# Optimization experiments

Measured on AMD Instinct MI355X. Metric: run time of the kernel, lower is better.

## Reference

```python
import jax, jax.numpy as jnp
import numpy as np

N_NODES = 50000
N_EDGES = 300000
NODE_DIM = 11
EDGE_DIM = 5
HID = 256
L = 4
G = 1024  # num graphs
BN_EPS = 1e-5


def setup_inputs() -> dict:
    key = jax.random.key(0)
    ks = jax.random.split(key, 24)
    s = 0.05
    inp = {
        "x": jax.random.normal(ks[0], (N_NODES, NODE_DIM), jnp.float32),
        "edge_index": jax.random.randint(ks[1], (2, N_EDGES), 0, N_NODES, jnp.int32),
        "edge_attr": jax.random.normal(ks[2], (N_EDGES, EDGE_DIM), jnp.float32),
        "batch": jnp.sort(jax.random.randint(ks[3], (N_NODES,), 0, G, jnp.int32)),
        # node encoder
        "enc_W": jax.random.normal(ks[4], (NODE_DIM, HID), jnp.float32) * s,
        "enc_b": jnp.zeros((HID,), jnp.float32),
        # per-layer GINE params (stacked over layers)
        "edge_W": jax.random.normal(ks[5], (L, EDGE_DIM, HID), jnp.float32) * s,
        "edge_b": jnp.zeros((L, HID), jnp.float32),
        "mlp_W1": jax.random.normal(ks[6], (L, HID, HID), jnp.float32) * s,
        "mlp_b1": jnp.zeros((L, HID), jnp.float32),
        "mlp_W2": jax.random.normal(ks[7], (L, HID, HID), jnp.float32) * s,
        "mlp_b2": jnp.zeros((L, HID), jnp.float32),
        "bn_g": jnp.ones((L, HID), jnp.float32),
        "bn_b": jnp.zeros((L, HID), jnp.float32),
        # head: 3*HID -> HID -> HID//2 -> 1
        "head_W1": jax.random.normal(ks[8], (3 * HID, HID), jnp.float32) * s,
        "head_b1": jnp.zeros((HID,), jnp.float32),
        "head_W2": jax.random.normal(ks[9], (HID, HID // 2), jnp.float32) * s,
        "head_b2": jnp.zeros((HID // 2,), jnp.float32),
        "head_W3": jax.random.normal(ks[10], (HID // 2, 1), jnp.float32) * s,
        "head_b3": jnp.zeros((1,), jnp.float32),
    }
    return inp


def _forward(x, edge_attr, enc_W, enc_b, edge_W, edge_b, mlp_W1, mlp_b1,
             mlp_W2, mlp_b2, bn_g, bn_b, head_W1, head_b1, head_W2, head_b2,
             head_W3, head_b3, edge_index, batch):
    n = x.shape[0]
    src, dst = edge_index[0], edge_index[1]  # messages flow src(j) -> dst(i)
    h = jax.nn.relu(x @ enc_W + enc_b)  # [N, HID]
    for l in range(L):
        e = edge_attr @ edge_W[l] + edge_b[l]                 # [E, HID]
        msg = jax.nn.relu(h[src] + e)                         # [E, HID]
        aggr = jax.ops.segment_sum(msg, dst, num_segments=n)  # [N, HID]
        z = h + aggr                                          # (1+eps)*h + aggr, eps=0
        z = jax.nn.relu(z @ mlp_W1[l] + mlp_b1[l]) @ mlp_W2[l] + mlp_b2[l]
        # BatchNorm over node dim (batch statistics)
        mu = jnp.mean(z, axis=0)
        var = jnp.var(z, axis=0)
        z = (z - mu) * jax.lax.rsqrt(var + BN_EPS) * bn_g[l] + bn_b[l]
        h = jax.nn.relu(z) + h  # residual
    # mean / add / max pooling per graph
    sums = jax.ops.segment_sum(h, batch, num_segments=G)      # [G, HID]
    cnt = jax.ops.segment_sum(jnp.ones((n, 1), h.dtype), batch, num_segments=G)
    mean = sums / jnp.maximum(cnt, 1.0)
    mx = jax.ops.segment_max(h, batch, num_segments=G)
    g = jnp.concatenate([mean, sums, mx], axis=1)             # [G, 3*HID]
    g = jax.nn.relu(g @ head_W1 + head_b1)
    g = jax.nn.relu(g @ head_W2 + head_b2)
    out = g @ head_W3 + head_b3
    return out.reshape(-1)  # [G]


def reference(x, edge_index, edge_attr, batch, enc_W, enc_b, edge_W, edge_b,
              mlp_W1, mlp_b1, mlp_W2, mlp_b2, bn_g, bn_b, head_W1, head_b1,
              head_W2, head_b2, head_W3, head_b3):
    return _forward(x, edge_attr, enc_W, enc_b, edge_W, edge_b, mlp_W1, mlp_b1,
                    mlp_W2, mlp_b2, bn_g, bn_b, head_W1, head_b1, head_W2,
                    head_b2, head_W3, head_b3, edge_index, batch)
```

## Files before the change

### kernel.cpp

```cpp
#include <hip/hip_runtime.h>

#define N_NODES 50000
#define N_EDGES 300000
#define G_GRAPHS 1024
#define HID 256
#define NLAYERS 4

typedef unsigned short ushort_t;
typedef __attribute__((ext_vector_type(8))) short bf16x8;
typedef __attribute__((ext_vector_type(8))) unsigned short u16x8;
typedef __attribute__((ext_vector_type(4))) float f32x4;

__device__ __forceinline__ float bf2f(ushort_t u) {
  unsigned int x = ((unsigned int)u) << 16;
  return __builtin_bit_cast(float, x);
}
__device__ __forceinline__ ushort_t f2bf(float f) {
  unsigned int x = __builtin_bit_cast(unsigned int, f);
  unsigned int lsb = (x >> 16) & 1u;
  x += 0x7fffu + lsb;
  return (ushort_t)(x >> 16);
}

__global__ __launch_bounds__(256) void k_encoder(const float* __restrict__ x,
    const float* __restrict__ W, const float* __restrict__ b,
    ushort_t* __restrict__ h, int n)
{
  int j = threadIdx.x;
  float wcol[11];
#pragma unroll
  for (int k = 0; k < 11; ++k) wcol[k] = W[k * HID + j];
  float bj = b[j];
  __shared__ float xs[8][11];
  int base = blockIdx.x * 8;
  if (j < 88) {
    int r = j / 11, k = j % 11;
    int row = base + r;
    if (row < n) xs[r][k] = x[row * 11 + k];
  }
  __syncthreads();
#pragma unroll
  for (int r = 0; r < 8; ++r) {
    int row = base + r;
    if (row >= n) break;
    float acc = bj;
#pragma unroll
    for (int k = 0; k < 11; ++k) acc += xs[r][k] * wcol[k];
    h[(size_t)row * HID + j] = f2bf(fmaxf(acc, 0.f));
  }
}

__global__ __launch_bounds__(256) void k_hist(const int* __restrict__ dst,
    int* __restrict__ offs, int E)
{
  int e = blockIdx.x * 256 + threadIdx.x;
  if (e < E) atomicAdd(&offs[dst[e]], 1);
}

__global__ __launch_bounds__(1024) void k_scanA(int* __restrict__ offs,
    int* __restrict__ btot, int n)
{
  __shared__ int wsum[16];
  int tid = threadIdx.x, lane = tid & 63, wid = tid >> 6;
  int idx = blockIdx.x * 1024 + tid;
  int v = (idx < n) ? offs[idx] : 0;
  int x = v;
#pragma unroll
  for (int off = 1; off < 64; off <<= 1) {
    int t = __shfl_up(x, off);
    if (lane >= off) x += t;
  }
  if (lane == 63) wsum[wid] = x;
  __syncthreads();
  if (wid == 0 && lane < 16) {
    int w = wsum[lane];
#pragma unroll
    for (int off = 1; off < 16; off <<= 1) {
      int t = __shfl_up(w, off);
      if (lane >= off) w += t;
    }
    wsum[lane] = w;
  }
  __syncthreads();
  int wbase = (wid == 0) ? 0 : wsum[wid - 1];
  if (idx < n) offs[idx] = wbase + x - v;
  if (tid == 0) btot[blockIdx.x] = wsum[15];
}

__global__ __launch_bounds__(64) void k_scanB(int* __restrict__ btot, int nb)
{
  int lane = threadIdx.x;
  int v = (lane < nb) ? btot[lane] : 0;
  int x = v;
#pragma unroll
  for (int off = 1; off < 64; off <<= 1) {
    int t = __shfl_up(x, off);
    if (lane >= off) x += t;
  }
  if (lane < nb) btot[lane] = x - v;
}

__global__ __launch_bounds__(1024) void k_scanC(int* __restrict__ offs,
    const int* __restrict__ btot, int n)
{
  int idx = blockIdx.x * 1024 + threadIdx.x;
  if (idx < n) offs[idx] += btot[blockIdx.x];
}

__global__ __launch_bounds__(256) void k_fill(const int* __restrict__ src,
    const int* __restrict__ dst, int* __restrict__ offs,
    int* __restrict__ esrc, ushort_t* __restrict__ eab,
    const float* __restrict__ ea, int E)
{
  int e = blockIdx.x * 256 + threadIdx.x;
  if (e < E) {
    int d = dst[e];
    int p = atomicAdd(&offs[d], 1);
    esrc[p] = src[e];
    const float* ep = ea + (size_t)e * 5;
    ushort4 lo = make_ushort4(f2bf(ep[0]), f2bf(ep[1]), f2bf(ep[2]), f2bf(ep[3]));
    ushort4 hi = make_ushort4(f2bf(ep[4]), 0, 0, 0);
    *(ushort4*)&eab[(size_t)p * 8] = lo;
    *(ushort4*)&eab[(size_t)p * 8 + 4] = hi;
  }
}

__global__ __launch_bounds__(256) void k_prep(const float* __restrict__ W,
    ushort_t* __restrict__ Wt)
{
  __shared__ float ld[16][257];
  int mat = blockIdx.y;
  int k0 = blockIdx.x * 16;
  const float* Wm = W + (size_t)mat * HID * HID;
  ushort_t* Wtm = Wt + (size_t)mat * HID * HID;
  int tid = threadIdx.x;
#pragma unroll
  for (int i = 0; i < 16; ++i) ld[i][tid] = Wm[(size_t)(k0 + i) * HID + tid];
  __syncthreads();
#pragma unroll
  for (int v = 0; v < 4; ++v) {
    ushort4 u = make_ushort4(f2bf(ld[v*4+0][tid]), f2bf(ld[v*4+1][tid]),
                             f2bf(ld[v*4+2][tid]), f2bf(ld[v*4+3][tid]));
    *(ushort4*)&Wtm[(size_t)tid * HID + k0 + v * 4] = u;
  }
}

__global__ __launch_bounds__(256) void k_prept(const float* __restrict__ W,
    ushort_t* __restrict__ Wt, int K, int N)
{
  int idx = blockIdx.x * 256 + threadIdx.x;
  if (idx >= K * N) return;
  int n = idx / K, k = idx % K;
  Wt[idx] = f2bf(W[(size_t)k * N + n]);
}

struct ev5 { ushort_t s0, s1, s2, s3, s4; };

__device__ __forceinline__ void edge_step(ev5 ev, ushort4 hv,
    const float4& w0, const float4& w1, const float4& w2, const float4& w3,
    const float4& w4, const float4& bi,
    float& ax, float& ay, float& az, float& aw)
{
  float v0 = bf2f(ev.s0), v1 = bf2f(ev.s1), v2 = bf2f(ev.s2),
        v3 = bf2f(ev.s3), v4 = bf2f(ev.s4);
  float m0 = bi.x, m1 = bi.y, m2 = bi.z, m3 = bi.w;
  m0 = fmaf(v0, w0.x, m0); m1 = fmaf(v0, w0.y, m1);
  m2 = fmaf(v0, w0.z, m2); m3 = fmaf(v0, w0.w, m3);
  m0 = fmaf(v1, w1.x, m0); m1 = fmaf(v1, w1.y, m1);
  m2 = fmaf(v1, w1.z, m2); m3 = fmaf(v1, w1.w, m3);
  m0 = fmaf(v2, w2.x, m0); m1 = fmaf(v2, w2.y, m1);
  m2 = fmaf(v2, w2.z, m2); m3 = fmaf(v2, w2.w, m3);
  m0 = fmaf(v3, w3.x, m0); m1 = fmaf(v3, w3.y, m1);
  m2 = fmaf(v3, w3.z, m2); m3 = fmaf(v3, w3.w, m3);
  m0 = fmaf(v4, w4.x, m0); m1 = fmaf(v4, w4.y, m1);
  m2 = fmaf(v4, w4.z, m2); m3 = fmaf(v4, w4.w, m3);
  m0 += bf2f(hv.x); m1 += bf2f(hv.y); m2 += bf2f(hv.z); m3 += bf2f(hv.w);
  ax += fmaxf(m0, 0.f); ay += fmaxf(m1, 0.f);
  az += fmaxf(m2, 0.f); aw += fmaxf(m3, 0.f);
}

__global__ __launch_bounds__(256) void k_gather(const ushort_t* __restrict__ h,
    const int* __restrict__ offs, const int* __restrict__ esrc,
    const ushort_t* __restrict__ eab, const float* __restrict__ eW,
    const float* __restrict__ eb, ushort_t* __restrict__ zin,
    float* __restrict__ stats, int n)
{
  int tid = threadIdx.x;
  if (blockIdx.x == 0) { stats[tid] = 0.f; stats[HID + tid] = 0.f; }
  int wave = tid >> 6, lane = tid & 63;
  int node = blockIdx.x * 4 + wave;
  int c4 = lane * 4;
  float4 w0 = *(const float4*)&eW[0 * HID + c4];
  float4 w1 = *(const float4*)&eW[1 * HID + c4];
  float4 w2 = *(const float4*)&eW[2 * HID + c4];
  float4 w3 = *(const float4*)&eW[3 * HID + c4];
  float4 w4 = *(const float4*)&eW[4 * HID + c4];
  float4 bi = *(const float4*)&eb[c4];
  if (node >= n) return;
  int lo = (node == 0) ? 0 : offs[node - 1];
  int hi = offs[node];
  ushort4 ho = *(const ushort4*)&h[(size_t)node * HID + c4];
  float ax = bf2f(ho.x), ay = bf2f(ho.y), az = bf2f(ho.z), aw = bf2f(ho.w);
  int p = lo;
  for (; p + 3 < hi; p += 4) {
    int s0 = esrc[p], s1 = esrc[p + 1], s2 = esrc[p + 2], s3 = esrc[p + 3];
    ev5 ea0 = *(const ev5*)&eab[(size_t)(p + 0) * 8];
    ev5 ea1 = *(const ev5*)&eab[(size_t)(p + 1) * 8];
    ev5 ea2 = *(const ev5*)&eab[(size_t)(p + 2) * 8];
    ev5 ea3 = *(const ev5*)&eab[(size_t)(p + 3) * 8];
    ushort4 h0 = *(const ushort4*)&h[(size_t)s0 * HID + c4];
    ushort4 h1 = *(const ushort4*)&h[(size_t)s1 * HID + c4];
    ushort4 h2 = *(const ushort4*)&h[(size_t)s2 * HID + c4];
    ushort4 h3 = *(const ushort4*)&h[(size_t)s3 * HID + c4];
    edge_step(ea0, h0, w0, w1, w2, w3, w4, bi, ax, ay, az, aw);
    edge_step(ea1, h1, w0, w1, w2, w3, w4, bi, ax, ay, az, aw);
    edge_step(ea2, h2, w0, w1, w2, w3, w4, bi, ax, ay, az, aw);
    edge_step(ea3, h3, w0, w1, w2, w3, w4, bi, ax, ay, az, aw);
  }
  for (; p < hi; ++p) {
    int s0 = esrc[p];
    ev5 ea0 = *(const ev5*)&eab[(size_t)p * 8];
    ushort4 h0 = *(const ushort4*)&h[(size_t)s0 * HID + c4];
    edge_step(ea0, h0, w0, w1, w2, w3, w4, bi, ax, ay, az, aw);
  }
  *(ushort4*)&zin[(size_t)node * HID + c4] =
      make_ushort4(f2bf(ax), f2bf(ay), f2bf(az), f2bf(aw));
}

__global__ __launch_bounds__(512, 1) void k_mlp(const ushort_t* __restrict__ A,
    const ushort_t* __restrict__ Wt1, const float* __restrict__ b1,
    const ushort_t* __restrict__ Wt2, const float* __restrict__ b2,
    ushort_t* __restrict__ out, float* __restrict__ stats, int M)
{
  __shared__ alignas(16) ushort_t w2L[65536];
  __shared__ alignas(16) ushort_t z1s[2][16 * 264];
  int tid = threadIdx.x;
  int wave = tid >> 6, lane = tid & 63;
  int m = lane & 15, quad = lane >> 4;
  int col0 = wave * 32;
  for (int c = tid; c < 8192; c += 512) {
    int f = c >> 6, l = c & 63;
    int ctg = f >> 3, kt = f & 7;
    int n = ctg * 16 + (l & 15);
    int k = kt * 32 + (l >> 4) * 8;
    *(u16x8*)&w2L[f * 512 + l * 8] = *(const u16x8*)(Wt2 + (size_t)n * HID + k);
  }
  bf16x8 w1f[2][8];
#pragma unroll
  for (int ct = 0; ct < 2; ++ct)
#pragma unroll
    for (int kt = 0; kt < 8; ++kt)
      w1f[ct][kt] = *(const bf16x8*)(
          Wt1 + (size_t)(col0 + ct * 16 + m) * HID + kt * 32 + quad * 8);
  float bv1[2] = {b1[col0 + m], b1[col0 + 16 + m]};
  float bv2[2] = {b2[col0 + m], b2[col0 + 16 + m]};
  float csum[2] = {0.f, 0.f}, csq[2] = {0.f, 0.f};
  int ntiles = M >> 4;
  int parity = 0;
  int ctg0 = wave * 2, ctg1 = wave * 2 + 1;
  __syncthreads();
  int t = blockIdx.x;
  bf16x8 af[8];
  if (t < ntiles) {
    const ushort_t* Ap = A + (size_t)(t * 16 + m) * HID + quad * 8;
#pragma unroll
    for (int kt = 0; kt < 8; ++kt) af[kt] = *(const bf16x8*)(Ap + kt * 32);
  }
  for (; t < ntiles; t += gridDim.x) {
    f32x4 a0 = (f32x4){0.f, 0.f, 0.f, 0.f};
    f32x4 a1 = (f32x4){0.f, 0.f, 0.f, 0.f};
#pragma unroll
    for (int kt = 0; kt < 8; ++kt) {
      a0 = __builtin_amdgcn_mfma_f32_16x16x32_bf16(af[kt], w1f[0][kt], a0, 0, 0, 0);
      a1 = __builtin_amdgcn_mfma_f32_16x16x32_bf16(af[kt], w1f[1][kt], a1, 0, 0, 0);
    }
    ushort_t* buf = z1s[parity];
#pragma unroll
    for (int reg = 0; reg < 4; ++reg) {
      int r = quad * 4 + reg;
      buf[r * 264 + col0 + m]      = f2bf(fmaxf(a0[reg] + bv1[0], 0.f));
      buf[r * 264 + col0 + 16 + m] = f2bf(fmaxf(a1[reg] + bv1[1], 0.f));
    }
    int tn = t + gridDim.x;
    bf16x8 afn[8];
    if (tn < ntiles) {
      const ushort_t* Ap = A + (size_t)(tn * 16 + m) * HID + quad * 8;
#pragma unroll
      for (int kt = 0; kt < 8; ++kt) afn[kt] = *(const bf16x8*)(Ap + kt * 32);
    }
    __syncthreads();
    f32x4 c0 = (f32x4){0.f, 0.f, 0.f, 0.f};
    f32x4 c1 = (f32x4){0.f, 0.f, 0.f, 0.f};
#pragma unroll
    for (int kt = 0; kt < 8; ++kt) {
      bf16x8 zf = *(const bf16x8*)&buf[m * 264 + kt * 32 + quad * 8];
      bf16x8 b0 = *(const bf16x8*)&w2L[(ctg0 * 8 + kt) * 512 + lane * 8];
      bf16x8 b1r = *(const bf16x8*)&w2L[(ctg1 * 8 + kt) * 512 + lane * 8];
      c0 = __builtin_amdgcn_mfma_f32_16x16x32_bf16(zf, b0, c0, 0, 0, 0);
      c1 = __builtin_amdgcn_mfma_f32_16x16x32_bf16(zf, b1r, c1, 0, 0, 0);
    }
    int rb = t * 16 + quad * 4;
#pragma unroll
    for (int reg = 0; reg < 4; ++reg) {
      float o0 = c0[reg] + bv2[0];
      float o1 = c1[reg] + bv2[1];
      out[(size_t)(rb + reg) * HID + col0 + m] = f2bf(o0);
      out[(size_t)(rb + reg) * HID + col0 + 16 + m] = f2bf(o1);
      csum[0] += o0; csq[0] = fmaf(o0, o0, csq[0]);
      csum[1] += o1; csq[1] = fmaf(o1, o1, csq[1]);
    }
#pragma unroll
    for (int kt = 0; kt < 8; ++kt) af[kt] = afn[kt];
    parity ^= 1;
  }
#pragma unroll
  for (int ct = 0; ct < 2; ++ct) {
    float s = csum[ct], q = csq[ct];
    s += __shfl_xor(s, 16); s += __shfl_xor(s, 32);
    q += __shfl_xor(q, 16); q += __shfl_xor(q, 32);
    if (quad == 0) {
      unsafeAtomicAdd(&stats[col0 + ct * 16 + m], s);
      unsafeAtomicAdd(&stats[HID + col0 + ct * 16 + m], q);
    }
  }
}

__global__ __launch_bounds__(256) void k_bn_apply(const ushort_t* __restrict__ z,
    const float* __restrict__ stats, const float* __restrict__ g,
    const float* __restrict__ b, ushort_t* __restrict__ h, int total4)
{
  int idx = blockIdx.x * 256 + threadIdx.x;
  if (idx >= total4) return;
  int col = (idx & 63) * 4;
  const float inv_n = 1.f / (float)N_NODES;
  float sc[4], sh[4];
#pragma unroll
  for (int c = 0; c < 4; ++c) {
    float mu = stats[col + c] * inv_n;
    float var = stats[HID + col + c] * inv_n - mu * mu;
    float rs = rsqrtf(var + 1e-5f);
    sc[c] = g[col + c] * rs;
    sh[c] = b[col + c] - mu * sc[c];
  }
  ushort4 zv = *(const ushort4*)(z + (size_t)idx * 4);
  ushort4 hv = *(const ushort4*)(h + (size_t)idx * 4);
  float o0 = fmaxf(fmaf(bf2f(zv.x), sc[0], sh[0]), 0.f) + bf2f(hv.x);
  float o1 = fmaxf(fmaf(bf2f(zv.y), sc[1], sh[1]), 0.f) + bf2f(hv.y);
  float o2 = fmaxf(fmaf(bf2f(zv.z), sc[2], sh[2]), 0.f) + bf2f(hv.z);
  float o3 = fmaxf(fmaf(bf2f(zv.w), sc[3], sh[3]), 0.f) + bf2f(hv.w);
  *(ushort4*)(h + (size_t)idx * 4) = make_ushort4(f2bf(o0), f2bf(o1), f2bf(o2), f2bf(o3));
}

__device__ __forceinline__ int lbound(const int* __restrict__ b, int n, int key) {
  int lo = 0, hi = n;
  while (lo < hi) {
    int mid = (lo + hi) >> 1;
    if (b[mid] < key) lo = mid + 1; else hi = mid;
  }
  return lo;
}

__global__ __launch_bounds__(256) void k_pool(const ushort_t* __restrict__ h,
    const int* __restrict__ batch, ushort_t* __restrict__ gf)
{
  int g = blockIdx.x, j = threadIdx.x;
  int lo = lbound(batch, N_NODES, g);
  int hi = lbound(batch, N_NODES, g + 1);
  float s = 0.f, mx = 0.f;
  int i = lo;
  for (; i + 1 < hi; i += 2) {
    float v0 = bf2f(h[(size_t)i * HID + j]);
    float v1 = bf2f(h[(size_t)(i + 1) * HID + j]);
    s += v0 + v1; mx = fmaxf(mx, fmaxf(v0, v1));
  }
  if (i < hi) {
    float v = bf2f(h[(size_t)i * HID + j]);
    s += v; mx = fmaxf(mx, v);
  }
  float cntv = fmaxf((float)(hi - lo), 1.f);
  size_t base = (size_t)g * 768;
  gf[base + j] = f2bf(s / cntv);
  gf[base + 256 + j] = f2bf(s);
  gf[base + 512 + j] = f2bf(mx);
}

template<int KT, int DO_RELU>
__global__ __launch_bounds__(256, 1) void k_head_gemm(const ushort_t* __restrict__ A,
    const ushort_t* __restrict__ Bt, const float* __restrict__ bias,
    ushort_t* __restrict__ out, int M, int N)
{
  const int K = KT * 32;
  int tid = threadIdx.x;
  int wave = tid >> 6, lane = tid & 63;
  int m = lane & 15, quad = lane >> 4;
  int col = (blockIdx.y * 4 + wave) * 16 + m;
  bf16x8 bfrag[KT];
#pragma unroll
  for (int kt = 0; kt < KT; ++kt)
    bfrag[kt] = *(const bf16x8*)(Bt + (size_t)col * K + kt * 32 + quad * 8);
  float bv = bias[col];
  int ntiles = M >> 4;
  for (int t = blockIdx.x; t < ntiles; t += gridDim.x) {
    const ushort_t* Ap = A + (size_t)(t * 16 + m) * K + quad * 8;
    bf16x8 af[KT];
#pragma unroll
    for (int kt = 0; kt < KT; ++kt) af[kt] = *(const bf16x8*)(Ap + kt * 32);
    f32x4 acc = (f32x4){0.f, 0.f, 0.f, 0.f};
#pragma unroll
    for (int kt = 0; kt < KT; ++kt)
      acc = __builtin_amdgcn_mfma_f32_16x16x32_bf16(af[kt], bfrag[kt], acc, 0, 0, 0);
    int rb = t * 16 + quad * 4;
#pragma unroll
    for (int reg = 0; reg < 4; ++reg) {
      float o = acc[reg] + bv;
      if (DO_RELU) o = fmaxf(o, 0.f);
      out[(size_t)(rb + reg) * N + col] = f2bf(o);
    }
  }
}

__global__ __launch_bounds__(256) void k_head_out(const ushort_t* __restrict__ g2,
    const float* __restrict__ W3, const float* __restrict__ b3,
    float* __restrict__ out)
{
  int wave = threadIdx.x >> 6, lane = threadIdx.x & 63;
  int g = blockIdx.x * 4 + wave;
  ushort2 v = *(const ushort2*)&g2[(size_t)g * 128 + lane * 2];
  float p = bf2f(v.x) * W3[lane * 2] + bf2f(v.y) * W3[lane * 2 + 1];
#pragma unroll
  for (int off = 32; off > 0; off >>= 1) p += __shfl_down(p, off);
  if (lane == 0) out[g] = p + b3[0];
}

extern "C" void kernel_launch(void* const* d_in, const int* in_sizes, int n_in,
                              void* d_out, int out_size, void* d_ws, size_t ws_size,
                              hipStream_t stream)
{
  const float* x     = (const float*)d_in[0];
  const int*   ei    = (const int*)d_in[1];
  const float* ea    = (const float*)d_in[2];
  const int*   batch = (const int*)d_in[3];
  const float* encW  = (const float*)d_in[4];
  const float* encB  = (const float*)d_in[5];
  const float* edgeW = (const float*)d_in[6];
  const float* edgeB = (const float*)d_in[7];
  const float* W1    = (const float*)d_in[8];
  const float* b1    = (const float*)d_in[9];
  const float* W2    = (const float*)d_in[10];
  const float* b2    = (const float*)d_in[11];
  const float* bng   = (const float*)d_in[12];
  const float* bnb   = (const float*)d_in[13];
  const float* hW1   = (const float*)d_in[14];
  const float* hb1   = (const float*)d_in[15];
  const float* hW2   = (const float*)d_in[16];
  const float* hb2   = (const float*)d_in[17];
  const float* hW3   = (const float*)d_in[18];
  const float* hb3   = (const float*)d_in[19];
  float* out = (float*)d_out;

  const size_t NH = (size_t)N_NODES * HID;
  char* base = (char*)d_ws;
  auto alloc = [&](size_t bytes) -> char* {
    char* p = base; base += (bytes + 63) & ~(size_t)63; return p;
  };
  float*    stats = (float*)alloc(512 * 4);
  int*      offs  = (int*)alloc(50001 * 4);
  int*      btot  = (int*)alloc(64 * 4);
  int*      esrc  = (int*)alloc((size_t)N_EDGES * 4);
  ushort_t* eab   = (ushort_t*)alloc((size_t)N_EDGES * 8 * 2);
  ushort_t* Wt1   = (ushort_t*)alloc((size_t)NLAYERS * HID * HID * 2);
  ushort_t* Wt2   = (ushort_t*)alloc((size_t)NLAYERS * HID * HID * 2);
  ushort_t* hW1t  = (ushort_t*)alloc((size_t)768 * 256 * 2);
  ushort_t* hW2t  = (ushort_t*)alloc((size_t)256 * 128 * 2);
  ushort_t* gf    = (ushort_t*)alloc((size_t)G_GRAPHS * 768 * 2);
  ushort_t* g1    = (ushort_t*)alloc((size_t)G_GRAPHS * 256 * 2);
  ushort_t* g2    = (ushort_t*)alloc((size_t)G_GRAPHS * 128 * 2);
  ushort_t* zin   = (ushort_t*)alloc(NH * 2);
  ushort_t* h     = (ushort_t*)alloc(NH * 2);

  const int* src = ei;
  const int* dst = ei + N_EDGES;

  hipMemsetAsync(offs, 0, 50001 * sizeof(int), stream);
  k_hist<<<(N_EDGES + 255) / 256, 256, 0, stream>>>(dst, offs, N_EDGES);
  const int NSB = (N_NODES + 1023) / 1024;
  k_scanA<<<NSB, 1024, 0, stream>>>(offs, btot, N_NODES);
  k_scanB<<<1, 64, 0, stream>>>(btot, NSB);
  k_scanC<<<NSB, 1024, 0, stream>>>(offs, btot, N_NODES);
  k_fill<<<(N_EDGES + 255) / 256, 256, 0, stream>>>(src, dst, offs, esrc, eab, ea, N_EDGES);
  k_prep<<<dim3(16, NLAYERS), 256, 0, stream>>>(W1, Wt1);
  k_prep<<<dim3(16, NLAYERS), 256, 0, stream>>>(W2, Wt2);
  k_prept<<<(768 * 256 + 255) / 256, 256, 0, stream>>>(hW1, hW1t, 768, 256);
  k_prept<<<(256 * 128 + 255) / 256, 256, 0, stream>>>(hW2, hW2t, 256, 128);

  k_encoder<<<(N_NODES + 7) / 8, 256, 0, stream>>>(x, encW, encB, h, N_NODES);

  for (int l = 0; l < NLAYERS; ++l) {
    k_gather<<<N_NODES / 4, 256, 0, stream>>>(
        h, offs, esrc, eab, edgeW + (size_t)l * 5 * HID, edgeB + (size_t)l * HID,
        zin, stats, N_NODES);
    k_mlp<<<256, 512, 0, stream>>>(
        zin, Wt1 + (size_t)l * HID * HID, b1 + (size_t)l * HID,
        Wt2 + (size_t)l * HID * HID, b2 + (size_t)l * HID, zin, stats, N_NODES);
    k_bn_apply<<<(N_NODES * HID / 4 + 255) / 256, 256, 0, stream>>>(
        zin, stats, bng + (size_t)l * HID, bnb + (size_t)l * HID, h, N_NODES * HID / 4);
  }

  k_pool<<<G_GRAPHS, 256, 0, stream>>>(h, batch, gf);
  k_head_gemm<24, 1><<<dim3(16, 4), 256, 0, stream>>>(gf, hW1t, hb1, g1, G_GRAPHS, 256);
  k_head_gemm<8, 1><<<dim3(16, 2), 256, 0, stream>>>(g1, hW2t, hb2, g2, G_GRAPHS, 128);
  k_head_out<<<G_GRAPHS / 4, 256, 0, stream>>>(g2, hW3, hb3, out);
}
```

Measured before the change: 620.0 us.

## Split per-node edge gather across two waves and merge small launches

```diff
diff --git a/kernel.cpp b/kernel.cpp
--- a/kernel.cpp
+++ b/kernel.cpp
@@ -87,24 +87,18 @@
   if (tid == 0) btot[blockIdx.x] = wsum[15];
 }
 
-__global__ __launch_bounds__(64) void k_scanB(int* __restrict__ btot, int nb)
-{
-  int lane = threadIdx.x;
-  int v = (lane < nb) ? btot[lane] : 0;
-  int x = v;
-#pragma unroll
-  for (int off = 1; off < 64; off <<= 1) {
-    int t = __shfl_up(x, off);
-    if (lane >= off) x += t;
-  }
-  if (lane < nb) btot[lane] = x - v;
-}
-
 __global__ __launch_bounds__(1024) void k_scanC(int* __restrict__ offs,
     const int* __restrict__ btot, int n)
 {
+  __shared__ int sbase;
+  if (threadIdx.x == 0) {
+    int s = 0;
+    for (int i = 0; i < blockIdx.x; ++i) s += btot[i];
+    sbase = s;
+  }
+  __syncthreads();
   int idx = blockIdx.x * 1024 + threadIdx.x;
-  if (idx < n) offs[idx] += btot[blockIdx.x];
+  if (idx < n) offs[idx] += sbase;
 }
 
 __global__ __launch_bounds__(256) void k_fill(const int* __restrict__ src,
@@ -125,14 +119,16 @@
   }
 }
 
-__global__ __launch_bounds__(256) void k_prep(const float* __restrict__ W,
-    ushort_t* __restrict__ Wt)
+__global__ __launch_bounds__(256) void k_prep(const float* __restrict__ W1,
+    const float* __restrict__ W2, ushort_t* __restrict__ Wt1,
+    ushort_t* __restrict__ Wt2)
 {
   __shared__ float ld[16][257];
-  int mat = blockIdx.y;
+  int mat = blockIdx.y & (NLAYERS - 1);
+  int which = blockIdx.y >> 2;
+  const float* Wm = (which ? W2 : W1) + (size_t)mat * HID * HID;
+  ushort_t* Wtm = (which ? Wt2 : Wt1) + (size_t)mat * HID * HID;
   int k0 = blockIdx.x * 16;
-  const float* Wm = W + (size_t)mat * HID * HID;
-  ushort_t* Wtm = Wt + (size_t)mat * HID * HID;
   int tid = threadIdx.x;
 #pragma unroll
   for (int i = 0; i < 16; ++i) ld[i][tid] = Wm[(size_t)(k0 + i) * HID + tid];
@@ -185,10 +181,13 @@
     const float* __restrict__ eb, ushort_t* __restrict__ zin,
     float* __restrict__ stats, int n)
 {
+  __shared__ float part[2][HID];
   int tid = threadIdx.x;
   if (blockIdx.x == 0) { stats[tid] = 0.f; stats[HID + tid] = 0.f; }
   int wave = tid >> 6, lane = tid & 63;
-  int node = blockIdx.x * 4 + wave;
+  int nloc = wave >> 1;
+  int half = wave & 1;
+  int node = blockIdx.x * 2 + nloc;
   int c4 = lane * 4;
   float4 w0 = *(const float4*)&eW[0 * HID + c4];
   float4 w1 = *(const float4*)&eW[1 * HID + c4];
@@ -196,35 +195,37 @@
   float4 w3 = *(const float4*)&eW[3 * HID + c4];
   float4 w4 = *(const float4*)&eW[4 * HID + c4];
   float4 bi = *(const float4*)&eb[c4];
-  if (node >= n) return;
   int lo = (node == 0) ? 0 : offs[node - 1];
   int hi = offs[node];
-  ushort4 ho = *(const ushort4*)&h[(size_t)node * HID + c4];
-  float ax = bf2f(ho.x), ay = bf2f(ho.y), az = bf2f(ho.z), aw = bf2f(ho.w);
-  int p = lo;
-  for (; p + 3 < hi; p += 4) {
-    int s0 = esrc[p], s1 = esrc[p + 1], s2 = esrc[p + 2], s3 = esrc[p + 3];
-    ev5 ea0 = *(const ev5*)&eab[(size_t)(p + 0) * 8];
-    ev5 ea1 = *(const ev5*)&eab[(size_t)(p + 1) * 8];
-    ev5 ea2 = *(const ev5*)&eab[(size_t)(p + 2) * 8];
-    ev5 ea3 = *(const ev5*)&eab[(size_t)(p + 3) * 8];
+  float ax = 0.f, ay = 0.f, az = 0.f, aw = 0.f;
+  int p = lo + half;
+  for (; p + 2 < hi; p += 4) {
+    int s0 = esrc[p], s1 = esrc[p + 2];
+    ev5 ea0 = *(const ev5*)&eab[(size_t)p * 8];
+    ev5 ea1 = *(const ev5*)&eab[(size_t)(p + 2) * 8];
     ushort4 h0 = *(const ushort4*)&h[(size_t)s0 * HID + c4];
     ushort4 h1 = *(const ushort4*)&h[(size_t)s1 * HID + c4];
-    ushort4 h2 = *(const ushort4*)&h[(size_t)s2 * HID + c4];
-    ushort4 h3 = *(const ushort4*)&h[(size_t)s3 * HID + c4];
     edge_step(ea0, h0, w0, w1, w2, w3, w4, bi, ax, ay, az, aw);
     edge_step(ea1, h1, w0, w1, w2, w3, w4, bi, ax, ay, az, aw);
-    edge_step(ea2, h2, w0, w1, w2, w3, w4, bi, ax, ay, az, aw);
-    edge_step(ea3, h3, w0, w1, w2, w3, w4, bi, ax, ay, az, aw);
-  }
-  for (; p < hi; ++p) {
+  }
+  if (p < hi) {
     int s0 = esrc[p];
     ev5 ea0 = *(const ev5*)&eab[(size_t)p * 8];
     ushort4 h0 = *(const ushort4*)&h[(size_t)s0 * HID + c4];
     edge_step(ea0, h0, w0, w1, w2, w3, w4, bi, ax, ay, az, aw);
   }
-  *(ushort4*)&zin[(size_t)node * HID + c4] =
-      make_ushort4(f2bf(ax), f2bf(ay), f2bf(az), f2bf(aw));
+  if (half == 1) {
+    *(float4*)&part[nloc][c4] = make_float4(ax, ay, az, aw);
+  }
+  __syncthreads();
+  if (half == 0) {
+    float4 pv = *(const float4*)&part[nloc][c4];
+    ushort4 ho = *(const ushort4*)&h[(size_t)node * HID + c4];
+    ax += pv.x + bf2f(ho.x); ay += pv.y + bf2f(ho.y);
+    az += pv.z + bf2f(ho.z); aw += pv.w + bf2f(ho.w);
+    *(ushort4*)&zin[(size_t)node * HID + c4] =
+        make_ushort4(f2bf(ax), f2bf(ay), f2bf(az), f2bf(aw));
+  }
 }
 
 __global__ __launch_bounds__(512, 1) void k_mlp(const ushort_t* __restrict__ A,
@@ -267,6 +268,12 @@
     for (int kt = 0; kt < 8; ++kt) af[kt] = *(const bf16x8*)(Ap + kt * 32);
   }
   for (; t < ntiles; t += gridDim.x) {
+    int tn = t + gridDim.x;
+    int tcl = (tn < ntiles) ? tn : t;
+    const ushort_t* Apn = A + (size_t)(tcl * 16 + m) * HID + quad * 8;
+    bf16x8 afn[8];
+#pragma unroll
+    for (int kt = 0; kt < 8; ++kt) afn[kt] = *(const bf16x8*)(Apn + kt * 32);
     f32x4 a0 = (f32x4){0.f, 0.f, 0.f, 0.f};
     f32x4 a1 = (f32x4){0.f, 0.f, 0.f, 0.f};
 #pragma unroll
@@ -280,13 +287,6 @@
       int r = quad * 4 + reg;
       buf[r * 264 + col0 + m]      = f2bf(fmaxf(a0[reg] + bv1[0], 0.f));
       buf[r * 264 + col0 + 16 + m] = f2bf(fmaxf(a1[reg] + bv1[1], 0.f));
-    }
-    int tn = t + gridDim.x;
-    bf16x8 afn[8];
-    if (tn < ntiles) {
-      const ushort_t* Ap = A + (size_t)(tn * 16 + m) * HID + quad * 8;
-#pragma unroll
-      for (int kt = 0; kt < 8; ++kt) afn[kt] = *(const bf16x8*)(Ap + kt * 32);
     }
     __syncthreads();
     f32x4 c0 = (f32x4){0.f, 0.f, 0.f, 0.f};
@@ -485,18 +485,16 @@
   k_hist<<<(N_EDGES + 255) / 256, 256, 0, stream>>>(dst, offs, N_EDGES);
   const int NSB = (N_NODES + 1023) / 1024;
   k_scanA<<<NSB, 1024, 0, stream>>>(offs, btot, N_NODES);
-  k_scanB<<<1, 64, 0, stream>>>(btot, NSB);
   k_scanC<<<NSB, 1024, 0, stream>>>(offs, btot, N_NODES);
   k_fill<<<(N_EDGES + 255) / 256, 256, 0, stream>>>(src, dst, offs, esrc, eab, ea, N_EDGES);
-  k_prep<<<dim3(16, NLAYERS), 256, 0, stream>>>(W1, Wt1);
-  k_prep<<<dim3(16, NLAYERS), 256, 0, stream>>>(W2, Wt2);
+  k_prep<<<dim3(16, 2 * NLAYERS), 256, 0, stream>>>(W1, W2, Wt1, Wt2);
   k_prept<<<(768 * 256 + 255) / 256, 256, 0, stream>>>(hW1, hW1t, 768, 256);
   k_prept<<<(256 * 128 + 255) / 256, 256, 0, stream>>>(hW2, hW2t, 256, 128);
 
   k_encoder<<<(N_NODES + 7) / 8, 256, 0, stream>>>(x, encW, encB, h, N_NODES);
 
   for (int l = 0; l < NLAYERS; ++l) {
-    k_gather<<<N_NODES / 4, 256, 0, stream>>>(
+    k_gather<<<N_NODES / 2, 256, 0, stream>>>(
         h, offs, esrc, eab, edgeW + (size_t)l * 5 * HID, edgeB + (size_t)l * HID,
         zin, stats, N_NODES);
     k_mlp<<<256, 512, 0, stream>>>(
```

Measured after the change: 626.1 us. No clear change (+1.0%).
